# Performance work log

Measured on AMD Instinct MI355X. Metric: run time of the kernel, lower is better.

Reference implementation:

```python
import jax, jax.numpy as jnp
import numpy as np
import math

DIM = 1024
B, S = 4, 2048

def setup_inputs() -> dict:
    key = jax.random.key(0)
    ks = jax.random.split(key, 4)
    scale = 1.0 / math.sqrt(DIM)
    X = jax.random.normal(ks[0], (B, S, DIM), dtype=jnp.float32)
    W_in = jax.random.normal(ks[1], (3 * DIM, DIM), dtype=jnp.float32) * scale
    b_in = jnp.zeros((3 * DIM,), dtype=jnp.float32)
    W_out = jax.random.normal(ks[2], (DIM, DIM), dtype=jnp.float32) * scale
    b_out = jnp.zeros((DIM,), dtype=jnp.float32)
    attention_mask = jnp.ones((B, 1, S), dtype=jnp.int32)
    return {"X": X, "attention_mask": attention_mask, "W_in": W_in,
            "b_in": b_in, "W_out": W_out, "b_out": b_out}

def reference(X, attention_mask, W_in, b_in, W_out, b_out):
    # in_proj: [B,S,3*DIM]
    qkv = jnp.einsum('bsd,ed->bse', X, W_in) + b_in
    Q, K, V = jnp.split(qkv, 3, axis=-1)
    # scores: [B,S,S]
    scores = jnp.einsum('bqd,bkd->bqk', Q, K)
    # masked_fill happens BEFORE the /sqrt(dim) scaling in the original
    scores = jnp.where(attention_mask == 0, jnp.float32(-1e20), scores)
    attn = jax.nn.softmax(scores / jnp.float32(math.sqrt(DIM)), axis=-1)
    # Dropout(0.1) treated as identity (eval-mode reference)
    out = jnp.einsum('bqk,bkd->bqd', attn, V)
    return jnp.einsum('bsd,od->bso', out, W_out) + b_out
```

## Files before the change

kernel.cpp:

```cpp
#include <hip/hip_runtime.h>
#include <stdint.h>

#define AS1 __attribute__((address_space(1)))
#define AS3 __attribute__((address_space(3)))

typedef __bf16 bf16x8 __attribute__((ext_vector_type(8)));
typedef float f32x16 __attribute__((ext_vector_type(16)));

__device__ __forceinline__ unsigned short f2bf(float f) {
  unsigned u = __float_as_uint(f);
  u += 0x7FFF + ((u >> 16) & 1);
  return (unsigned short)(u >> 16);
}

__global__ __launch_bounds__(256) void cast_all_kernel(const float* __restrict__ X,
                                                       const float* __restrict__ Wi,
                                                       const float* __restrict__ Wo,
                                                       unsigned short* __restrict__ out) {
  const int c1 = 2097152;
  const int c2 = 786432;
  const int c3 = 262144;
  int i = blockIdx.x * 256 + threadIdx.x;
  if (i >= c1 + c2 + c3) return;
  const float* src;
  int j = i;
  if (i < c1) src = X;
  else if (i < c1 + c2) { src = Wi; j = i - c1; }
  else { src = Wo; j = i - c1 - c2; }
  float4 v = reinterpret_cast<const float4*>(src)[j];
  ushort4 o;
  o.x = f2bf(v.x); o.y = f2bf(v.y); o.z = f2bf(v.z); o.w = f2bf(v.w);
  reinterpret_cast<ushort4*>(out)[i] = o;
}

template<int MODE>
__global__ __launch_bounds__(512, 2) void gemmQ(
    const unsigned short* __restrict__ A, long lda, long strideA,
    const unsigned short* __restrict__ B, long ldb, long strideB,
    void* __restrict__ Cv, long ldc, long strideC,
    const float* __restrict__ bias, const int* __restrict__ mask,
    float* __restrict__ sums, unsigned short* __restrict__ vt, int K) {
  __shared__ unsigned short sAll[65536];
  char* sBase = (char*)sAll;
  const int t = threadIdx.x;
  const int lane = t & 63;
  const int wave = t >> 6;

  const int nx = gridDim.x;
  const int nwg = nx * gridDim.y;
  int orig = blockIdx.y * nx + blockIdx.x;
  int q = nwg >> 3, r8 = nwg & 7;
  int xcd = orig & 7, idx = orig >> 3;
  int wg = (xcd < r8 ? xcd * (q + 1) : r8 * (q + 1) + (xcd - r8) * q) + idx;
  const int bx = wg % nx, by = wg / nx, bz = blockIdx.z;

  const unsigned short* Ab = A + (size_t)bz * strideA + (size_t)by * 256 * lda;
  const unsigned short* Bb = B + (size_t)bz * strideB + (size_t)bx * 256 * ldb;

  const int srow = t >> 2;
  const int scol = ((t & 3) ^ ((srow >> 2) & 3)) << 3;
  const unsigned short* aS = Ab + (size_t)srow * lda + scol;
  const unsigned short* bS = Bb + (size_t)srow * ldb + scol;

  auto stage = [&](int tk, int s) {
    char* base = sBase + s * 32768 + wave * 1024;
    const unsigned short* ap = aS + tk * 32;
    const unsigned short* bp = bS + tk * 32;
#pragma unroll
    for (int l = 0; l < 2; l++)
      __builtin_amdgcn_global_load_lds((AS1 void*)(ap + (size_t)(l * 128) * lda),
                                       (AS3 void*)(base + l * 8192), 16, 0, 0);
#pragma unroll
    for (int l = 0; l < 2; l++)
      __builtin_amdgcn_global_load_lds((AS1 void*)(bp + (size_t)(l * 128) * ldb),
                                       (AS3 void*)(base + 16384 + l * 8192), 16, 0, 0);
  };

  const int NT = K >> 5;

  f32x16 acc[4][2];
#pragma unroll
  for (int i = 0; i < 4; i++)
#pragma unroll
    for (int j = 0; j < 2; j++)
#pragma unroll
      for (int r = 0; r < 16; r++) acc[i][j][r] = 0.f;

  const int wm = (wave >> 2) << 7;
  const int wn = (wave & 3) << 6;
  const int r31 = lane & 31;
  const int half = lane >> 5;
  const int swz = (r31 >> 2) & 3;
  int offC[2];
#pragma unroll
  for (int ks = 0; ks < 2; ks++)
    offC[ks] = ((((ks << 1) + half) ^ swz) << 4);
  int rowA[4], rowB[2];
#pragma unroll
  for (int i = 0; i < 4; i++) rowA[i] = (wm + 32 * i + r31) << 6;
#pragma unroll
  for (int j = 0; j < 2; j++) rowB[j] = (wn + 32 * j + r31) << 6;

  stage(0, 0);
  stage(1, 1);
  stage(2, 2);
  asm volatile("s_waitcnt vmcnt(8)" ::: "memory");
  __builtin_amdgcn_sched_barrier(0);
  __builtin_amdgcn_s_barrier();
  __builtin_amdgcn_sched_barrier(0);

  for (int tk = 0; tk < NT; ++tk) {
    const char* sa = sBase + (tk & 3) * 32768;
    const char* sb = sa + 16384;
    bf16x8 aq0[2], aq1[2], aq2[2], aq3[2], bq0[2], bq1[2];
#pragma unroll
    for (int ks = 0; ks < 2; ks++) {
      bq0[ks] = *reinterpret_cast<const bf16x8*>(sb + rowB[0] + offC[ks]);
      bq1[ks] = *reinterpret_cast<const bf16x8*>(sb + rowB[1] + offC[ks]);
      aq0[ks] = *reinterpret_cast<const bf16x8*>(sa + rowA[0] + offC[ks]);
      aq1[ks] = *reinterpret_cast<const bf16x8*>(sa + rowA[1] + offC[ks]);
      aq2[ks] = *reinterpret_cast<const bf16x8*>(sa + rowA[2] + offC[ks]);
      aq3[ks] = *reinterpret_cast<const bf16x8*>(sa + rowA[3] + offC[ks]);
    }
    __builtin_amdgcn_s_setprio(1);
#pragma unroll
    for (int ks = 0; ks < 2; ks++) {
      acc[0][0] = __builtin_amdgcn_mfma_f32_32x32x16_bf16(aq0[ks], bq0[ks], acc[0][0], 0, 0, 0);
      acc[0][1] = __builtin_amdgcn_mfma_f32_32x32x16_bf16(aq0[ks], bq1[ks], acc[0][1], 0, 0, 0);
      acc[1][0] = __builtin_amdgcn_mfma_f32_32x32x16_bf16(aq1[ks], bq0[ks], acc[1][0], 0, 0, 0);
      acc[1][1] = __builtin_amdgcn_mfma_f32_32x32x16_bf16(aq1[ks], bq1[ks], acc[1][1], 0, 0, 0);
      acc[2][0] = __builtin_amdgcn_mfma_f32_32x32x16_bf16(aq2[ks], bq0[ks], acc[2][0], 0, 0, 0);
      acc[2][1] = __builtin_amdgcn_mfma_f32_32x32x16_bf16(aq2[ks], bq1[ks], acc[2][1], 0, 0, 0);
      acc[3][0] = __builtin_amdgcn_mfma_f32_32x32x16_bf16(aq3[ks], bq0[ks], acc[3][0], 0, 0, 0);
      acc[3][1] = __builtin_amdgcn_mfma_f32_32x32x16_bf16(aq3[ks], bq1[ks], acc[3][1], 0, 0, 0);
    }
    __builtin_amdgcn_s_setprio(0);
    if (tk == NT - 1) break;
    __builtin_amdgcn_sched_barrier(0);
    if (tk + 2 < NT) { asm volatile("s_waitcnt vmcnt(4)" ::: "memory"); }
    else             { asm volatile("s_waitcnt vmcnt(0)" ::: "memory"); }
    __builtin_amdgcn_sched_barrier(0);
    __builtin_amdgcn_s_barrier();
    __builtin_amdgcn_sched_barrier(0);
    if (tk + 3 < NT) stage(tk + 3, (tk + 3) & 3);
  }

  const int* mrow = (MODE == 2) ? (mask + (size_t)bz * 2048) : nullptr;
  const bool vblock = (MODE == 1) && (bx >= 8);

#pragma unroll
  for (int i = 0; i < 4; i++) {
    int gmb = by * 256 + wm + i * 32;
    float rs[16];
    if (MODE == 2) {
#pragma unroll
      for (int r = 0; r < 16; r++) rs[r] = 0.f;
    }
#pragma unroll
    for (int j = 0; j < 2; j++) {
      int gn = bx * 256 + wn + j * 32 + r31;
      float bv = (MODE == 1) ? bias[gn] : 0.0f;
      if (MODE == 1 && vblock) {
        int b = gmb >> 11;
        int sbase = gmb & 2047;
        int d = gn - 2048;
        unsigned short* vp = vt + (size_t)b * 1024 * 2048 + (size_t)d * 2048 + sbase + 4 * half;
#pragma unroll
        for (int qd = 0; qd < 4; qd++) {
          ushort4 o;
          o.x = f2bf(acc[i][j][4 * qd + 0] + bv);
          o.y = f2bf(acc[i][j][4 * qd + 1] + bv);
          o.z = f2bf(acc[i][j][4 * qd + 2] + bv);
          o.w = f2bf(acc[i][j][4 * qd + 3] + bv);
          *reinterpret_cast<ushort4*>(vp + 8 * qd) = o;
        }
      } else {
        bool msk = (MODE == 2) ? (mrow[gn] == 0) : false;
#pragma unroll
        for (int r = 0; r < 16; r++) {
          int row = (r & 3) + 8 * (r >> 2) + 4 * half;
          float val = acc[i][j][r] + bv;
          size_t off = (size_t)bz * strideC + (size_t)(gmb + row) * ldc + gn;
          if (MODE == 2) {
            if (msk) val = -1e20f;
            val = __expf(val * 0.03125f);
            rs[r] += val;
            ((unsigned short*)Cv)[off] = f2bf(val);
          } else {
            ((unsigned short*)Cv)[off] = f2bf(val);
          }
        }
      }
    }
    if (MODE == 2) {
      float* srowp = sums + (size_t)bz * 2048;
#pragma unroll
      for (int r = 0; r < 16; r++) {
        float v = rs[r];
#pragma unroll
        for (int o = 16; o >= 1; o >>= 1) v += __shfl_xor(v, o, 64);
        if (r31 == 0) {
          int row = (r & 3) + 8 * (r >> 2) + 4 * half;
          atomicAdd(&srowp[gmb + row], v);
        }
      }
    }
  }
}

template<int MODE>
__global__ __launch_bounds__(256, 2) void gemm_bt128(
    const unsigned short* __restrict__ A, long lda, long strideA,
    const unsigned short* __restrict__ B, long ldb, long strideB,
    void* __restrict__ Cv, long ldc, long strideC,
    const float* __restrict__ bias, const int* __restrict__ mask,
    float* __restrict__ sums, unsigned short* __restrict__ vt, int K) {
  __shared__ unsigned short sA[128 * 64];
  __shared__ unsigned short sB[128 * 64];
  const int t = threadIdx.x;
  const int lane = t & 63;
  const int wave = t >> 6;

  const unsigned short* Ab = A + (size_t)blockIdx.z * strideA + (size_t)blockIdx.y * 128 * lda;
  const unsigned short* Bb = B + (size_t)blockIdx.z * strideB + (size_t)blockIdx.x * 128 * ldb;

  const int srow = t >> 3;
  const int schunk = (t & 7) ^ ((srow >> 1) & 7);
  const unsigned short* aptr = Ab + (size_t)srow * lda + schunk * 8;
  const unsigned short* bptr = Bb + (size_t)srow * ldb + schunk * 8;
  char* ldsA0 = (char*)&sA[0] + wave * 1024;
  char* ldsB0 = (char*)&sB[0] + wave * 1024;

  f32x16 acc[2][2];
#pragma unroll
  for (int i = 0; i < 2; i++)
#pragma unroll
    for (int j = 0; j < 2; j++)
#pragma unroll
      for (int r = 0; r < 16; r++) acc[i][j][r] = 0.f;

  const int wm = (wave >> 1) * 64;
  const int wn = (wave & 1) * 64;
  const int r31 = lane & 31;
  const int half = lane >> 5;
  const int swz = (r31 >> 1) & 7;

  int offA[2][4], offB[2][4];
#pragma unroll
  for (int i = 0; i < 2; i++)
#pragma unroll
    for (int s = 0; s < 4; s++) {
      offA[i][s] = (wm + i * 32 + r31) * 128 + (((2 * s + half) ^ swz) * 16);
      offB[i][s] = (wn + i * 32 + r31) * 128 + (((2 * s + half) ^ swz) * 16);
    }

  for (int k0 = 0; k0 < K; k0 += 64) {
    __syncthreads();
#pragma unroll
    for (int o = 0; o < 4; o++) {
      __builtin_amdgcn_global_load_lds((AS1 void*)(aptr + (size_t)o * 32 * lda + k0),
                                       (AS3 void*)(ldsA0 + o * 4096), 16, 0, 0);
      __builtin_amdgcn_global_load_lds((AS1 void*)(bptr + (size_t)o * 32 * ldb + k0),
                                       (AS3 void*)(ldsB0 + o * 4096), 16, 0, 0);
    }
    __syncthreads();
#pragma unroll
    for (int s = 0; s < 4; s++) {
      bf16x8 af[2], bfv[2];
#pragma unroll
      for (int i = 0; i < 2; i++) {
        af[i]  = *reinterpret_cast<const bf16x8*>((const char*)sA + offA[i][s]);
        bfv[i] = *reinterpret_cast<const bf16x8*>((const char*)sB + offB[i][s]);
      }
#pragma unroll
      for (int i = 0; i < 2; i++)
#pragma unroll
        for (int j = 0; j < 2; j++)
          acc[i][j] = __builtin_amdgcn_mfma_f32_32x32x16_bf16(af[i], bfv[j], acc[i][j], 0, 0, 0);
    }
  }

#pragma unroll
  for (int i = 0; i < 2; i++) {
    int gmb = blockIdx.y * 128 + wm + i * 32;
    float inv_r[16];
    if (MODE == 3) {
#pragma unroll
      for (int r = 0; r < 16; r++) {
        int row = (r & 3) + 8 * (r >> 2) + 4 * half;
        inv_r[r] = 1.0f / sums[(size_t)blockIdx.z * 2048 + gmb + row];
      }
    }
#pragma unroll
    for (int j = 0; j < 2; j++) {
      int gn = blockIdx.x * 128 + wn + j * 32 + r31;
      float bv = (MODE == 0) ? bias[gn] : 0.0f;
#pragma unroll
      for (int r = 0; r < 16; r++) {
        int row = (r & 3) + 8 * (r >> 2) + 4 * half;
        float val = acc[i][j][r] + bv;
        size_t off = (size_t)blockIdx.z * strideC + (size_t)(gmb + row) * ldc + gn;
        if (MODE == 3) {
          ((unsigned short*)Cv)[off] = f2bf(val * inv_r[r]);
        } else {
          ((float*)Cv)[off] = val;
        }
      }
    }
  }
}

extern "C" void kernel_launch(void* const* d_in, const int* in_sizes, int n_in,
                              void* d_out, int out_size, void* d_ws, size_t ws_size,
                              hipStream_t stream) {
  const float* X = (const float*)d_in[0];
  const int* mask = (const int*)d_in[1];
  const float* W_in = (const float*)d_in[2];
  const float* b_in = (const float*)d_in[3];
  const float* W_out = (const float*)d_in[4];
  const float* b_out = (const float*)d_in[5];
  float* out = (float*)d_out;

  const int S = 2048, D = 1024;
  char* w = (char*)d_ws;
  unsigned short* Xb  = (unsigned short*)w;
  unsigned short* Wib = (unsigned short*)(w + 16777216);
  unsigned short* Wob = (unsigned short*)(w + 16777216 + 6291456);
  unsigned short* QK  = (unsigned short*)(w + 25165824);
  unsigned short* P   = (unsigned short*)(w + 58720256);
  unsigned short* Vt  = (unsigned short*)(w + 92274688);
  float*          sums = (float*)(w + 109051904);
  unsigned short* Ob  = Xb;

  hipMemsetAsync(sums, 0, 8192 * sizeof(float), stream);

  cast_all_kernel<<<12288, 256, 0, stream>>>(X, W_in, W_out, Xb);

  gemmQ<1><<<dim3(12, 32, 1), 512, 0, stream>>>(
      Xb, D, 0, Wib, D, 0, QK, 2048, 0, b_in, nullptr, nullptr, Vt, D);
  gemmQ<2><<<dim3(8, 8, 4), 512, 0, stream>>>(
      QK, 2048, (long)S * 2048, QK + 1024, 2048, (long)S * 2048,
      P, S, (long)S * S, nullptr, mask, sums, nullptr, D);
  gemm_bt128<3><<<dim3(8, 16, 4), 256, 0, stream>>>(
      P, S, (long)S * S, Vt, S, (long)D * S,
      Ob, D, (long)S * D, nullptr, nullptr, sums, nullptr, S);
  gemm_bt128<0><<<dim3(8, 64, 1), 256, 0, stream>>>(
      Ob, D, 0, Wob, D, 0, out, D, 0, b_out, nullptr, nullptr, nullptr, D);
}
```

Baseline: 308.0 us.

## Split GEMM main loop into interleaved half-tile phases with separate A/B staging

The 256x256 GEMM main loop is restructured to process two K-tiles per iteration, each split into two half-phases with a barrier-separated LDS read/MFMA pattern. The A and B global-to-LDS loads are issued separately between phases so memory traffic is spread across the compute. Each half-phase reads fewer operand registers, which cuts register pressure, but the number of barriers per tile goes up. Separately, the cast kernel becomes a grid-stride loop with 2048 blocks instead of one thread per element chunk.

```diff
diff --git a/kernel.cpp b/kernel.cpp
--- a/kernel.cpp
+++ b/kernel.cpp
@@ -20,21 +20,22 @@
   const int c1 = 2097152;
   const int c2 = 786432;
   const int c3 = 262144;
-  int i = blockIdx.x * 256 + threadIdx.x;
-  if (i >= c1 + c2 + c3) return;
-  const float* src;
-  int j = i;
-  if (i < c1) src = X;
-  else if (i < c1 + c2) { src = Wi; j = i - c1; }
-  else { src = Wo; j = i - c1 - c2; }
-  float4 v = reinterpret_cast<const float4*>(src)[j];
-  ushort4 o;
-  o.x = f2bf(v.x); o.y = f2bf(v.y); o.z = f2bf(v.z); o.w = f2bf(v.w);
-  reinterpret_cast<ushort4*>(out)[i] = o;
+  const int total = c1 + c2 + c3;
+  for (int i = blockIdx.x * 256 + threadIdx.x; i < total; i += 2048 * 256) {
+    const float* src;
+    int j = i;
+    if (i < c1) src = X;
+    else if (i < c1 + c2) { src = Wi; j = i - c1; }
+    else { src = Wo; j = i - c1 - c2; }
+    float4 v = reinterpret_cast<const float4*>(src)[j];
+    ushort4 o;
+    o.x = f2bf(v.x); o.y = f2bf(v.y); o.z = f2bf(v.z); o.w = f2bf(v.w);
+    reinterpret_cast<ushort4*>(out)[i] = o;
+  }
 }
 
 template<int MODE>
-__global__ __launch_bounds__(512, 2) void gemmQ(
+__global__ __launch_bounds__(512, 2) void gemm8p(
     const unsigned short* __restrict__ A, long lda, long strideA,
     const unsigned short* __restrict__ B, long ldb, long strideB,
     void* __restrict__ Cv, long ldc, long strideC,
@@ -62,21 +63,25 @@
   const unsigned short* aS = Ab + (size_t)srow * lda + scol;
   const unsigned short* bS = Bb + (size_t)srow * ldb + scol;
 
-  auto stage = [&](int tk, int s) {
-    char* base = sBase + s * 32768 + wave * 1024;
+  auto stageA = [&](int tk) {
+    char* base = sBase + (tk & 3) * 32768 + wave * 1024;
     const unsigned short* ap = aS + tk * 32;
-    const unsigned short* bp = bS + tk * 32;
 #pragma unroll
     for (int l = 0; l < 2; l++)
       __builtin_amdgcn_global_load_lds((AS1 void*)(ap + (size_t)(l * 128) * lda),
                                        (AS3 void*)(base + l * 8192), 16, 0, 0);
+  };
+  auto stageB = [&](int tk) {
+    char* base = sBase + (tk & 3) * 32768 + 16384 + wave * 1024;
+    const unsigned short* bp = bS + tk * 32;
 #pragma unroll
     for (int l = 0; l < 2; l++)
       __builtin_amdgcn_global_load_lds((AS1 void*)(bp + (size_t)(l * 128) * ldb),
-                                       (AS3 void*)(base + 16384 + l * 8192), 16, 0, 0);
+                                       (AS3 void*)(base + l * 8192), 16, 0, 0);
   };
 
   const int NT = K >> 5;
+  const int NTH = NT >> 1;
 
   f32x16 acc[4][2];
 #pragma unroll
@@ -101,49 +106,83 @@
 #pragma unroll
   for (int j = 0; j < 2; j++) rowB[j] = (wn + 32 * j + r31) << 6;
 
-  stage(0, 0);
-  stage(1, 1);
-  stage(2, 2);
+  auto RD2 = [&](bf16x8 (&d)[2], const char* s, int row) {
+    d[0] = *reinterpret_cast<const bf16x8*>(s + row + offC[0]);
+    d[1] = *reinterpret_cast<const bf16x8*>(s + row + offC[1]);
+  };
+  auto MF8 = [&](f32x16& c00, f32x16& c01, f32x16& c10, f32x16& c11,
+                 bf16x8 (&xa)[2], bf16x8 (&xb)[2], bf16x8 (&b0)[2], bf16x8 (&b1)[2]) {
+#pragma unroll
+    for (int ks = 0; ks < 2; ks++) {
+      c00 = __builtin_amdgcn_mfma_f32_32x32x16_bf16(xa[ks], b0[ks], c00, 0, 0, 0);
+      c01 = __builtin_amdgcn_mfma_f32_32x32x16_bf16(xa[ks], b1[ks], c01, 0, 0, 0);
+      c10 = __builtin_amdgcn_mfma_f32_32x32x16_bf16(xb[ks], b0[ks], c10, 0, 0, 0);
+      c11 = __builtin_amdgcn_mfma_f32_32x32x16_bf16(xb[ks], b1[ks], c11, 0, 0, 0);
+    }
+  };
+
+#define SB0 __builtin_amdgcn_sched_barrier(0)
+#define BAR __builtin_amdgcn_s_barrier()
+#define LGKM0 asm volatile("s_waitcnt lgkmcnt(0)" ::: "memory")
+
+  stageA(0); stageB(0);
+  stageA(1); stageB(1);
+  stageA(2); stageB(2);
   asm volatile("s_waitcnt vmcnt(8)" ::: "memory");
-  __builtin_amdgcn_sched_barrier(0);
-  __builtin_amdgcn_s_barrier();
-  __builtin_amdgcn_sched_barrier(0);
-
-  for (int tk = 0; tk < NT; ++tk) {
-    const char* sa = sBase + (tk & 3) * 32768;
-    const char* sb = sa + 16384;
-    bf16x8 aq0[2], aq1[2], aq2[2], aq3[2], bq0[2], bq1[2];
-#pragma unroll
-    for (int ks = 0; ks < 2; ks++) {
-      bq0[ks] = *reinterpret_cast<const bf16x8*>(sb + rowB[0] + offC[ks]);
-      bq1[ks] = *reinterpret_cast<const bf16x8*>(sb + rowB[1] + offC[ks]);
-      aq0[ks] = *reinterpret_cast<const bf16x8*>(sa + rowA[0] + offC[ks]);
-      aq1[ks] = *reinterpret_cast<const bf16x8*>(sa + rowA[1] + offC[ks]);
-      aq2[ks] = *reinterpret_cast<const bf16x8*>(sa + rowA[2] + offC[ks]);
-      aq3[ks] = *reinterpret_cast<const bf16x8*>(sa + rowA[3] + offC[ks]);
-    }
+  SB0; BAR; SB0;
+
+  for (int it = 0; it < NTH; ++it) {
+    const int t0 = 2 * it, t1 = t0 + 1;
+    const char* sa0 = sBase + (t0 & 3) * 32768; const char* sb0 = sa0 + 16384;
+    const char* sa1 = sBase + (t1 & 3) * 32768; const char* sb1 = sa1 + 16384;
+    const int tS0 = t0 + 3, tS1 = t0 + 4;
+    bf16x8 bq0[2], bq1[2], a0[2], a1[2];
+
+    RD2(bq0, sb0, rowB[0]); RD2(bq1, sb0, rowB[1]);
+    RD2(a0, sa0, rowA[0]);  RD2(a1, sa0, rowA[1]);
+    if (tS0 < NT) stageA(tS0);
+    SB0; BAR; LGKM0; SB0;
     __builtin_amdgcn_s_setprio(1);
-#pragma unroll
-    for (int ks = 0; ks < 2; ks++) {
-      acc[0][0] = __builtin_amdgcn_mfma_f32_32x32x16_bf16(aq0[ks], bq0[ks], acc[0][0], 0, 0, 0);
-      acc[0][1] = __builtin_amdgcn_mfma_f32_32x32x16_bf16(aq0[ks], bq1[ks], acc[0][1], 0, 0, 0);
-      acc[1][0] = __builtin_amdgcn_mfma_f32_32x32x16_bf16(aq1[ks], bq0[ks], acc[1][0], 0, 0, 0);
-      acc[1][1] = __builtin_amdgcn_mfma_f32_32x32x16_bf16(aq1[ks], bq1[ks], acc[1][1], 0, 0, 0);
-      acc[2][0] = __builtin_amdgcn_mfma_f32_32x32x16_bf16(aq2[ks], bq0[ks], acc[2][0], 0, 0, 0);
-      acc[2][1] = __builtin_amdgcn_mfma_f32_32x32x16_bf16(aq2[ks], bq1[ks], acc[2][1], 0, 0, 0);
-      acc[3][0] = __builtin_amdgcn_mfma_f32_32x32x16_bf16(aq3[ks], bq0[ks], acc[3][0], 0, 0, 0);
-      acc[3][1] = __builtin_amdgcn_mfma_f32_32x32x16_bf16(aq3[ks], bq1[ks], acc[3][1], 0, 0, 0);
-    }
+    MF8(acc[0][0], acc[0][1], acc[1][0], acc[1][1], a0, a1, bq0, bq1);
     __builtin_amdgcn_s_setprio(0);
-    if (tk == NT - 1) break;
-    __builtin_amdgcn_sched_barrier(0);
-    if (tk + 2 < NT) { asm volatile("s_waitcnt vmcnt(4)" ::: "memory"); }
-    else             { asm volatile("s_waitcnt vmcnt(0)" ::: "memory"); }
-    __builtin_amdgcn_sched_barrier(0);
-    __builtin_amdgcn_s_barrier();
-    __builtin_amdgcn_sched_barrier(0);
-    if (tk + 3 < NT) stage(tk + 3, (tk + 3) & 3);
-  }
+    SB0; BAR; SB0;
+
+    RD2(a0, sa0, rowA[2]); RD2(a1, sa0, rowA[3]);
+    if (tS0 < NT) stageB(tS0);
+    SB0; BAR; LGKM0; SB0;
+    __builtin_amdgcn_s_setprio(1);
+    MF8(acc[2][0], acc[2][1], acc[3][0], acc[3][1], a0, a1, bq0, bq1);
+    __builtin_amdgcn_s_setprio(0);
+    SB0;
+    if (tS0 < NT) { asm volatile("s_waitcnt vmcnt(8)" ::: "memory"); }
+    else          { asm volatile("s_waitcnt vmcnt(0)" ::: "memory"); }
+    SB0; BAR; SB0;
+
+    RD2(bq0, sb1, rowB[0]); RD2(bq1, sb1, rowB[1]);
+    RD2(a0, sa1, rowA[0]);  RD2(a1, sa1, rowA[1]);
+    if (tS1 < NT) stageA(tS1);
+    SB0; BAR; LGKM0; SB0;
+    __builtin_amdgcn_s_setprio(1);
+    MF8(acc[0][0], acc[0][1], acc[1][0], acc[1][1], a0, a1, bq0, bq1);
+    __builtin_amdgcn_s_setprio(0);
+    SB0; BAR; SB0;
+
+    RD2(a0, sa1, rowA[2]); RD2(a1, sa1, rowA[3]);
+    if (tS1 < NT) stageB(tS1);
+    SB0; BAR; LGKM0; SB0;
+    __builtin_amdgcn_s_setprio(1);
+    MF8(acc[2][0], acc[2][1], acc[3][0], acc[3][1], a0, a1, bq0, bq1);
+    __builtin_amdgcn_s_setprio(0);
+    SB0;
+    if (it < NTH - 1) {
+      if (tS1 < NT) { asm volatile("s_waitcnt vmcnt(8)" ::: "memory"); }
+      else          { asm volatile("s_waitcnt vmcnt(4)" ::: "memory"); }
+      SB0; BAR; SB0;
+    }
+  }
+#undef SB0
+#undef BAR
+#undef LGKM0
 
   const int* mrow = (MODE == 2) ? (mask + (size_t)bz * 2048) : nullptr;
   const bool vblock = (MODE == 1) && (bx >= 8);
@@ -334,11 +373,11 @@
 
   hipMemsetAsync(sums, 0, 8192 * sizeof(float), stream);
 
-  cast_all_kernel<<<12288, 256, 0, stream>>>(X, W_in, W_out, Xb);
-
-  gemmQ<1><<<dim3(12, 32, 1), 512, 0, stream>>>(
+  cast_all_kernel<<<2048, 256, 0, stream>>>(X, W_in, W_out, Xb);
+
+  gemm8p<1><<<dim3(12, 32, 1), 512, 0, stream>>>(
       Xb, D, 0, Wib, D, 0, QK, 2048, 0, b_in, nullptr, nullptr, Vt, D);
-  gemmQ<2><<<dim3(8, 8, 4), 512, 0, stream>>>(
+  gemm8p<2><<<dim3(8, 8, 4), 512, 0, stream>>>(
       QK, 2048, (long)S * 2048, QK + 1024, 2048, (long)S * 2048,
       P, S, (long)S * S, nullptr, mask, sums, nullptr, D);
   gemm_bt128<3><<<dim3(8, 16, 4), 256, 0, stream>>>(
```

New measurement: 309.1 us. No clear change (+0.4%).
